# Kernel optimization log

Hardware: AMD Instinct MI355X
Metric: run time of the kernel (lower is better)

The kernel has to match this reference:

```python
import jax, jax.numpy as jnp
import numpy as np

SHIFTS = (1, 2, 4, 8)  # exponential strategy, num_shifts=4

B, L, D = 2, 2048, 2048
CAT = D * (1 + 2 * len(SHIFTS))  # 18432


def setup_inputs() -> dict:
    key = jax.random.key(0)
    kx, kw, kb = jax.random.split(key, 3)
    x = jax.random.normal(kx, (B, L, D), dtype=jnp.float32)
    # nn.Linear(cat_dim, dim_out) weight is [dim_out, cat_dim]; store as [cat_dim, dim_out] transposed for matmul
    W = jax.random.normal(kw, (D, CAT), dtype=jnp.float32) * (1.0 / np.sqrt(CAT))
    b = jax.random.normal(kb, (D,), dtype=jnp.float32) * 0.01
    return {"x": x, "W": W, "b": b}


def reference(x, W, b):
    # x: [B, L, D]; W: [dim_out, cat_dim]; b: [dim_out]
    glo = jnp.mean(x, axis=1, keepdims=True)  # [B, 1, D] global context
    feats = [jax.nn.silu(x)]
    for s in SHIFTS:
        rg = jnp.roll(glo, s, axis=-1)          # [B, 1, D]
        xg = x * rg                              # [B, L, D]
        feats.append(jax.nn.silu(xg))            # inner(s)
        rx = jnp.roll(x, s, axis=-1)
        feats.append(xg - rx * glo)              # wedge(s)
    mixed = jnp.concatenate(feats, axis=-1)      # [B, L, cat_dim]
    out = jnp.einsum('blc,oc->blo', mixed, W) + b
    return out
```

## Files before the change

kernel.cpp:

```cpp
#include <hip/hip_runtime.h>
#include <stdint.h>

#define DDIM 2048
#define LDIM 2048
#define BDIM 2
#define CATK 18432
#define MDIM 4096
#define NDIM 2048
#define KGEMM 12288
#define KCHUNK 6144

typedef short bf16x8 __attribute__((ext_vector_type(8)));
typedef float f32x4 __attribute__((ext_vector_type(4)));
typedef unsigned short u16x8 __attribute__((ext_vector_type(8)));

__device__ __forceinline__ unsigned short f2bf(float f) {
  uint32_t u = __float_as_uint(f);
  return (unsigned short)((u + 0x7fffu + ((u >> 16) & 1u)) >> 16);
}
__device__ __forceinline__ float silu_f(float v) { return v / (1.0f + __expf(-v)); }

__device__ __forceinline__ void async16(const void* g, void* l) {
  __builtin_amdgcn_global_load_lds(
      (const __attribute__((address_space(1))) uint32_t*)(uintptr_t)g,
      (__attribute__((address_space(3))) uint32_t*)(uintptr_t)l, 16, 0, 0);
}

__global__ __launch_bounds__(256) void glo_partial(const float* __restrict__ x,
                                                   float* __restrict__ part) {
  int g = blockIdx.x;
  int dc = g & 7, sl = (g >> 3) & 15, b = g >> 7;
  int d = dc * 256 + threadIdx.x;
  const float* p = x + ((size_t)b * LDIM + (size_t)sl * 128) * DDIM + d;
  float s = 0.f;
  #pragma unroll 8
  for (int i = 0; i < 128; ++i) s += p[(size_t)i * DDIM];
  part[(size_t)(b * 16 + sl) * DDIM + d] = s;
}

__global__ __launch_bounds__(256) void glo_final(const float* __restrict__ part,
                                                 float* __restrict__ glo) {
  int idx = blockIdx.x * 256 + threadIdx.x;
  int b = idx >> 11, d = idx & 2047;
  float s = 0.f;
  #pragma unroll
  for (int i = 0; i < 16; ++i) s += part[(size_t)(b * 16 + i) * DDIM + d];
  glo[idx] = s * (1.0f / (float)LDIM);
}

__global__ __launch_bounds__(256) void conv_w5(const float* __restrict__ W,
                                               unsigned short* __restrict__ Wcat) {
  int k = blockIdx.x;
  int o = blockIdx.y;
  int srcb = (k == 0) ? 0 : (2 * k - 1);
  const float* src = W + (size_t)o * CATK + srcb * 2048 + threadIdx.x * 8;
  f32x4 a = *(const f32x4*)src;
  f32x4 c = *(const f32x4*)(src + 4);
  u16x8 v;
  v[0] = f2bf(a[0]); v[1] = f2bf(a[1]); v[2] = f2bf(a[2]); v[3] = f2bf(a[3]);
  v[4] = f2bf(c[0]); v[5] = f2bf(c[1]); v[6] = f2bf(c[2]); v[7] = f2bf(c[3]);
  size_t dst = (size_t)o * KGEMM + k * 2048 + threadIdx.x * 8;
  *(u16x8*)(Wcat + dst) = v;
  *(u16x8*)(Wcat + (size_t)2048 * KGEMM + dst) = v;
}

__global__ __launch_bounds__(256) void fold_w(const float* __restrict__ W,
                                              const float* __restrict__ glo,
                                              unsigned short* __restrict__ Wcat) {
  __shared__ float ws[4][2048];
  __shared__ float gsh[2048];
  int o = blockIdx.x, b = blockIdx.y;
  const float* gb = glo + (size_t)b * 2048;
  for (int i = threadIdx.x; i < 512; i += 256) {
    *(f32x4*)&gsh[i * 4] = *(const f32x4*)&gb[i * 4];
    #pragma unroll
    for (int j = 0; j < 4; ++j)
      *(f32x4*)&ws[j][i * 4] =
          *(const f32x4*)(W + (size_t)o * CATK + (2 + 2 * j) * 2048 + i * 4);
  }
  __syncthreads();
  int d0 = threadIdx.x * 8;
  u16x8 out;
  #pragma unroll
  for (int e = 0; e < 8; ++e) {
    int d = d0 + e;
    float v = 0.f;
    #pragma unroll
    for (int j = 0; j < 4; ++j) {
      int s = 1 << j;
      int dm = (d - s) & 2047, dp = (d + s) & 2047;
      v += ws[j][d] * gsh[dm] - ws[j][dp] * gsh[dp];
    }
    out[e] = f2bf(v);
  }
  *(u16x8*)(Wcat + ((size_t)b * 2048 + o) * KGEMM + 10240 + d0) = out;
}

__global__ __launch_bounds__(256) void build_mixed(const float* __restrict__ x,
                                                   const float* __restrict__ glo,
                                                   unsigned short* __restrict__ mixed) {
  __shared__ float xs[DDIM];
  __shared__ float gs[DDIM];
  int row = blockIdx.x;
  int b = row >> 11;
  const float* xr = x + (size_t)row * DDIM;
  const float* gr = glo + (size_t)b * DDIM;
  for (int i = threadIdx.x; i < DDIM / 4; i += 256) {
    *(f32x4*)&xs[i * 4] = *(const f32x4*)&xr[i * 4];
    *(f32x4*)&gs[i * 4] = *(const f32x4*)&gr[i * 4];
  }
  __syncthreads();
  unsigned short* mr = mixed + (size_t)row * KGEMM;
  int d0 = threadIdx.x * 8;
  u16x8 o0, oi[4], xb;
  #pragma unroll
  for (int j = 0; j < 8; ++j) {
    int d = d0 + j;
    float xv = xs[d];
    o0[j] = f2bf(silu_f(xv));
    xb[j] = f2bf(xv);
    #pragma unroll
    for (int si = 0; si < 4; ++si) {
      int s = 1 << si;
      int dm = (d - s) & (DDIM - 1);
      oi[si][j] = f2bf(silu_f(xv * gs[dm]));
    }
  }
  *(u16x8*)(mr + d0) = o0;
  #pragma unroll
  for (int si = 0; si < 4; ++si)
    *(u16x8*)(mr + (size_t)(1 + si) * DDIM + d0) = oi[si];
  *(u16x8*)(mr + (size_t)10240 + d0) = xb;
}

#define BAR() __builtin_amdgcn_s_barrier()
#define SCHEDB() __builtin_amdgcn_sched_barrier(0)
#define WAIT_VM4() asm volatile("s_waitcnt vmcnt(4)" ::: "memory")
#define WAIT_VM0() asm volatile("s_waitcnt vmcnt(0)" ::: "memory")
#define WAIT_LGKM0() asm volatile("s_waitcnt lgkmcnt(0)" ::: "memory")

#define STAGE_A(S, H, KREL)                                            \
  do {                                                                 \
    const unsigned short* g_ = gA + (size_t)((H)*128) * KGEMM + (KREL);\
    unsigned short* l_ = stA + ((S)*2 + (H)) * 8192;                   \
    async16(g_, l_);                                                   \
    async16(g_ + (size_t)8 * KGEMM, l_ + 512);                         \
  } while (0)

#define STAGE_B(S, H, KREL)                                            \
  do {                                                                 \
    const unsigned short* g_ = gB + (size_t)((H)*128) * KGEMM + (KREL);\
    unsigned short* l_ = stB + ((S)*2 + (H)) * 8192;                   \
    async16(g_, l_);                                                   \
    async16(g_ + (size_t)8 * KGEMM, l_ + 512);                         \
  } while (0)

#define LOAD_A(S, MH)                                                        \
  do {                                                                       \
    _Pragma("unroll") for (int mi = 0; mi < 4; ++mi) {                       \
      ra[mi][0] = *(const bf16x8*)(pA + (S)*16384 + ((MH)*64 + mi*16)*64 + sl0); \
      ra[mi][1] = *(const bf16x8*)(pA + (S)*16384 + ((MH)*64 + mi*16)*64 + sl1); \
    }                                                                        \
  } while (0)

#define LOAD_B(S, NH, RB)                                                    \
  do {                                                                       \
    _Pragma("unroll") for (int nj = 0; nj < 2; ++nj) {                       \
      RB[nj][0] = *(const bf16x8*)(pB + (S)*16384 + ((NH)*32 + nj*16)*64 + sl0); \
      RB[nj][1] = *(const bf16x8*)(pB + (S)*16384 + ((NH)*32 + nj*16)*64 + sl1); \
    }                                                                        \
  } while (0)

#define MFMA_QUAD(MH, NH, RB)                                                \
  do {                                                                       \
    __builtin_amdgcn_s_setprio(1);                                           \
    _Pragma("unroll") for (int kk = 0; kk < 2; ++kk)                         \
      _Pragma("unroll") for (int mi = 0; mi < 4; ++mi)                       \
        _Pragma("unroll") for (int nj = 0; nj < 2; ++nj)                     \
          acc[(MH)*4 + mi][(NH)*2 + nj] = __builtin_amdgcn_mfma_f32_16x16x32_bf16( \
              ra[mi][kk], RB[nj][kk], acc[(MH)*4 + mi][(NH)*2 + nj], 0, 0, 0);     \
    __builtin_amdgcn_s_setprio(0);                                           \
  } while (0)

__global__ __launch_bounds__(512, 2) void gemm256(const unsigned short* __restrict__ A,
                                                  const unsigned short* __restrict__ Bw,
                                                  const float* __restrict__ bias,
                                                  float* __restrict__ out0,
                                                  float* __restrict__ out1) {
  extern __shared__ unsigned short lds[];
  unsigned short* ldsA = lds;
  unsigned short* ldsB = lds + 32768;

  int bid = blockIdx.x;
  int swz = (bid & 7) * 32 + (bid >> 3);
  int kc = swz >> 7;
  int rem = swz & 127;
  int mt = rem >> 3, nt = rem & 7;
  size_t kbase = (size_t)kc * KCHUNK;

  int tid = threadIdx.x;
  int wave = tid >> 6, lane = tid & 63;
  int wr = wave >> 2, wcol = wave & 3;
  int lrow = lane & 15, kq = lane >> 4, r3 = lrow & 7;
  int rIn8 = lane >> 3;
  int scOff = ((lane & 7) ^ rIn8) * 8;
  int wv16 = wave * 16;

  const unsigned short* gA = A + (size_t)(mt * 256 + wv16 + rIn8) * KGEMM + kbase + scOff;
  const unsigned short* gB = Bw + (size_t)(mt >= 8 ? 2048 : 0) * KGEMM +
                             (size_t)(nt * 256 + wv16 + rIn8) * KGEMM + kbase + scOff;
  unsigned short* stA = ldsA + wv16 * 64;
  unsigned short* stB = ldsB + wv16 * 64;

  const unsigned short* pA = ldsA + wr * 8192 + lrow * 64;
  const unsigned short* pB = ldsB + (wcol >> 1) * 8192 + ((wcol & 1) * 64 + lrow) * 64;
  int sl0 = (kq ^ r3) * 8, sl1 = ((kq + 4) ^ r3) * 8;

  f32x4 acc[8][4];
  #pragma unroll
  for (int i = 0; i < 8; ++i)
    #pragma unroll
    for (int j = 0; j < 4; ++j) acc[i][j] = (f32x4)0.f;
  bf16x8 ra[4][2], rb0[2][2], rb1[2][2];

  STAGE_B(0, 0, 0); STAGE_B(0, 1, 0);
  STAGE_A(0, 0, 0); STAGE_A(0, 1, 0);
  STAGE_B(1, 0, 64); STAGE_B(1, 1, 64);
  WAIT_VM4(); SCHEDB();
  BAR(); SCHEDB();

  for (int t = 0; t < 47; ++t) {
    size_t k0 = (size_t)t * 128;
    LOAD_A(0, 0); LOAD_B(0, 0, rb0);
    STAGE_A(1, 0, k0 + 64);
    BAR(); WAIT_LGKM0(); SCHEDB();
    MFMA_QUAD(0, 0, rb0);
    SCHEDB(); BAR(); SCHEDB();
    LOAD_B(0, 1, rb1);
    STAGE_A(1, 1, k0 + 64);
    BAR(); WAIT_LGKM0(); SCHEDB();
    MFMA_QUAD(0, 1, rb1);
    SCHEDB(); BAR(); SCHEDB();
    LOAD_A(0, 1);
    STAGE_B(0, 0, k0 + 128);
    BAR(); WAIT_LGKM0(); SCHEDB();
    MFMA_QUAD(1, 1, rb1);
    SCHEDB(); BAR(); SCHEDB();
    STAGE_B(0, 1, k0 + 128);
    BAR(); SCHEDB();
    MFMA_QUAD(1, 0, rb0);
    WAIT_VM4(); SCHEDB(); BAR(); SCHEDB();
    LOAD_A(1, 0); LOAD_B(1, 0, rb0);
    STAGE_A(0, 0, k0 + 128);
    BAR(); WAIT_LGKM0(); SCHEDB();
    MFMA_QUAD(0, 0, rb0);
    SCHEDB(); BAR(); SCHEDB();
    LOAD_B(1, 1, rb1);
    STAGE_A(0, 1, k0 + 128);
    BAR(); WAIT_LGKM0(); SCHEDB();
    MFMA_QUAD(0, 1, rb1);
    SCHEDB(); BAR(); SCHEDB();
    LOAD_A(1, 1);
    STAGE_B(1, 0, k0 + 192);
    BAR(); WAIT_LGKM0(); SCHEDB();
    MFMA_QUAD(1, 1, rb1);
    SCHEDB(); BAR(); SCHEDB();
    STAGE_B(1, 1, k0 + 192);
    BAR(); SCHEDB();
    MFMA_QUAD(1, 0, rb0);
    WAIT_VM4(); SCHEDB(); BAR(); SCHEDB();
  }

  {
    size_t k0 = (size_t)47 * 128;
    LOAD_A(0, 0); LOAD_B(0, 0, rb0);
    STAGE_A(1, 0, k0 + 64);
    BAR(); WAIT_LGKM0(); SCHEDB();
    MFMA_QUAD(0, 0, rb0);
    SCHEDB(); BAR(); SCHEDB();
    LOAD_B(0, 1, rb1);
    STAGE_A(1, 1, k0 + 64);
    BAR(); WAIT_LGKM0(); SCHEDB();
    MFMA_QUAD(0, 1, rb1);
    SCHEDB(); BAR(); SCHEDB();
    LOAD_A(0, 1);
    BAR(); WAIT_LGKM0(); SCHEDB();
    MFMA_QUAD(1, 1, rb1);
    SCHEDB(); BAR(); SCHEDB();
    BAR(); SCHEDB();
    MFMA_QUAD(1, 0, rb0);
    WAIT_VM0(); SCHEDB(); BAR(); SCHEDB();
    LOAD_A(1, 0); LOAD_B(1, 0, rb0);
    BAR(); WAIT_LGKM0(); SCHEDB();
    MFMA_QUAD(0, 0, rb0);
    SCHEDB(); BAR(); SCHEDB();
    LOAD_B(1, 1, rb1);
    BAR(); WAIT_LGKM0(); SCHEDB();
    MFMA_QUAD(0, 1, rb1);
    SCHEDB(); BAR(); SCHEDB();
    LOAD_A(1, 1);
    BAR(); WAIT_LGKM0(); SCHEDB();
    MFMA_QUAD(1, 1, rb1);
    SCHEDB(); BAR(); SCHEDB();
    MFMA_QUAD(1, 0, rb0);
  }

  float* dst = kc ? out1 : out0;
  float bv[4];
  #pragma unroll
  for (int J = 0; J < 4; ++J)
    bv[J] = kc ? 0.f : bias[nt * 256 + wcol * 64 + J * 16 + lrow];
  #pragma unroll
  for (int I = 0; I < 8; ++I) {
    int row0 = mt * 256 + wr * 128 + I * 16 + kq * 4;
    #pragma unroll
    for (int J = 0; J < 4; ++J) {
      int col = nt * 256 + wcol * 64 + J * 16 + lrow;
      #pragma unroll
      for (int r = 0; r < 4; ++r)
        dst[(size_t)(row0 + r) * NDIM + col] = acc[I][J][r] + bv[J];
    }
  }
}

__global__ __launch_bounds__(256) void combine(float* __restrict__ out,
                                               const float* __restrict__ p1) {
  size_t n = (size_t)MDIM * NDIM / 4;
  size_t stride = (size_t)gridDim.x * 256;
  for (size_t i = (size_t)blockIdx.x * 256 + threadIdx.x; i < n; i += stride) {
    f32x4 a = ((const f32x4*)out)[i];
    f32x4 c = ((const f32x4*)p1)[i];
    ((f32x4*)out)[i] = a + c;
  }
}

extern "C" void kernel_launch(void* const* d_in, const int* in_sizes, int n_in,
                              void* d_out, int out_size, void* d_ws, size_t ws_size,
                              hipStream_t stream) {
  const float* x = (const float*)d_in[0];
  const float* W = (const float*)d_in[1];
  const float* b = (const float*)d_in[2];
  float* out = (float*)d_out;

  uint8_t* ws = (uint8_t*)d_ws;
  size_t offWcat = 0;
  size_t szWcat = (size_t)2 * NDIM * KGEMM * 2;
  size_t offMx = offWcat + szWcat;
  size_t szMx = (size_t)MDIM * KGEMM * 2;
  size_t offGlo = offMx + szMx;
  size_t szGlo = (size_t)BDIM * DDIM * 4;
  size_t offPart = offGlo + szGlo;
  size_t szPart = (size_t)BDIM * 16 * DDIM * 4;
  size_t offP1 = offPart + szPart;
  size_t szP1 = (size_t)MDIM * NDIM * 4;
  if (ws_size < offP1 + szP1) return;

  unsigned short* Wcat = (unsigned short*)(ws + offWcat);
  unsigned short* Mx = (unsigned short*)(ws + offMx);
  float* glo = (float*)(ws + offGlo);
  float* part = (float*)(ws + offPart);
  float* P1 = (float*)(ws + offP1);

  hipFuncSetAttribute((const void*)gemm256, hipFuncAttributeMaxDynamicSharedMemorySize,
                      131072);

  hipLaunchKernelGGL(glo_partial, dim3(256), dim3(256), 0, stream, x, part);
  hipLaunchKernelGGL(glo_final, dim3(16), dim3(256), 0, stream, part, glo);
  hipLaunchKernelGGL(conv_w5, dim3(5, 2048), dim3(256), 0, stream, W, Wcat);
  hipLaunchKernelGGL(fold_w, dim3(2048, 2), dim3(256), 0, stream, W, glo, Wcat);
  hipLaunchKernelGGL(build_mixed, dim3(4096), dim3(256), 0, stream, x, glo, Mx);

  hipLaunchKernelGGL(gemm256, dim3(256), dim3(512), 131072, stream, Mx, Wcat, b, out, P1);
  hipLaunchKernelGGL(combine, dim3(2048), dim3(256), 0, stream, out, P1);
}
```

Baseline: 295.5 us.

## Burst all LDS fragment reads per stage and merge fold_w batches

The GEMM main loop now issues all A and B fragment reads from LDS at the start of each stage into separate register sets (raA, raB, rb0, rb1). It then waits with partial lgkmcnt counts (12, 8, 0) so MFMAs can start while later reads are still in flight, replacing the serialized load-wait-compute steps. Separately, fold_w handles both batches in one block, so each W slice is read from memory once instead of twice. The extra fragment registers raise register pressure under the 512-thread, 2-block launch bound, and the partial-wait counts depend on how the compiler orders the LDS reads.

```diff
diff --git a/kernel.cpp b/kernel.cpp
--- a/kernel.cpp
+++ b/kernel.cpp
@@ -68,11 +68,11 @@
                                               const float* __restrict__ glo,
                                               unsigned short* __restrict__ Wcat) {
   __shared__ float ws[4][2048];
-  __shared__ float gsh[2048];
-  int o = blockIdx.x, b = blockIdx.y;
-  const float* gb = glo + (size_t)b * 2048;
+  __shared__ float g2[2][2048];
+  int o = blockIdx.x;
   for (int i = threadIdx.x; i < 512; i += 256) {
-    *(f32x4*)&gsh[i * 4] = *(const f32x4*)&gb[i * 4];
+    *(f32x4*)&g2[0][i * 4] = *(const f32x4*)&glo[i * 4];
+    *(f32x4*)&g2[1][i * 4] = *(const f32x4*)&glo[2048 + i * 4];
     #pragma unroll
     for (int j = 0; j < 4; ++j)
       *(f32x4*)&ws[j][i * 4] =
@@ -80,20 +80,23 @@
   }
   __syncthreads();
   int d0 = threadIdx.x * 8;
-  u16x8 out;
-  #pragma unroll
-  for (int e = 0; e < 8; ++e) {
-    int d = d0 + e;
-    float v = 0.f;
-    #pragma unroll
-    for (int j = 0; j < 4; ++j) {
-      int s = 1 << j;
-      int dm = (d - s) & 2047, dp = (d + s) & 2047;
-      v += ws[j][d] * gsh[dm] - ws[j][dp] * gsh[dp];
+  #pragma unroll
+  for (int b = 0; b < 2; ++b) {
+    u16x8 outv;
+    #pragma unroll
+    for (int e = 0; e < 8; ++e) {
+      int d = d0 + e;
+      float v = 0.f;
+      #pragma unroll
+      for (int j = 0; j < 4; ++j) {
+        int s = 1 << j;
+        int dm = (d - s) & 2047, dp = (d + s) & 2047;
+        v += ws[j][d] * g2[b][dm] - ws[j][dp] * g2[b][dp];
+      }
+      outv[e] = f2bf(v);
     }
-    out[e] = f2bf(v);
-  }
-  *(u16x8*)(Wcat + ((size_t)b * 2048 + o) * KGEMM + 10240 + d0) = out;
+    *(u16x8*)(Wcat + ((size_t)b * 2048 + o) * KGEMM + 10240 + d0) = outv;
+  }
 }
 
 __global__ __launch_bounds__(256) void build_mixed(const float* __restrict__ x,
@@ -137,7 +140,7 @@
 #define SCHEDB() __builtin_amdgcn_sched_barrier(0)
 #define WAIT_VM4() asm volatile("s_waitcnt vmcnt(4)" ::: "memory")
 #define WAIT_VM0() asm volatile("s_waitcnt vmcnt(0)" ::: "memory")
-#define WAIT_LGKM0() asm volatile("s_waitcnt lgkmcnt(0)" ::: "memory")
+#define WAIT_LGKM(N) asm volatile("s_waitcnt lgkmcnt(" #N ")" ::: "memory")
 
 #define STAGE_A(S, H, KREL)                                            \
   do {                                                                 \
@@ -155,11 +158,11 @@
     async16(g_ + (size_t)8 * KGEMM, l_ + 512);                         \
   } while (0)
 
-#define LOAD_A(S, MH)                                                        \
+#define LOAD_A(S, MH, RA)                                                    \
   do {                                                                       \
     _Pragma("unroll") for (int mi = 0; mi < 4; ++mi) {                       \
-      ra[mi][0] = *(const bf16x8*)(pA + (S)*16384 + ((MH)*64 + mi*16)*64 + sl0); \
-      ra[mi][1] = *(const bf16x8*)(pA + (S)*16384 + ((MH)*64 + mi*16)*64 + sl1); \
+      RA[mi][0] = *(const bf16x8*)(pA + (S)*16384 + ((MH)*64 + mi*16)*64 + sl0); \
+      RA[mi][1] = *(const bf16x8*)(pA + (S)*16384 + ((MH)*64 + mi*16)*64 + sl1); \
     }                                                                        \
   } while (0)
 
@@ -171,15 +174,23 @@
     }                                                                        \
   } while (0)
 
-#define MFMA_QUAD(MH, NH, RB)                                                \
+#define MFMA_QUAD(MH, NH, RA, RB)                                            \
   do {                                                                       \
     __builtin_amdgcn_s_setprio(1);                                           \
     _Pragma("unroll") for (int kk = 0; kk < 2; ++kk)                         \
       _Pragma("unroll") for (int mi = 0; mi < 4; ++mi)                       \
         _Pragma("unroll") for (int nj = 0; nj < 2; ++nj)                     \
           acc[(MH)*4 + mi][(NH)*2 + nj] = __builtin_amdgcn_mfma_f32_16x16x32_bf16( \
-              ra[mi][kk], RB[nj][kk], acc[(MH)*4 + mi][(NH)*2 + nj], 0, 0, 0);     \
+              RA[mi][kk], RB[nj][kk], acc[(MH)*4 + mi][(NH)*2 + nj], 0, 0, 0);     \
     __builtin_amdgcn_s_setprio(0);                                           \
+  } while (0)
+
+#define BURST_READS(S)                                                       \
+  do {                                                                       \
+    LOAD_A(S, 0, raA); SCHEDB();                                             \
+    LOAD_B(S, 0, rb0); SCHEDB();                                             \
+    LOAD_B(S, 1, rb1); SCHEDB();                                             \
+    LOAD_A(S, 1, raB); SCHEDB();                                             \
   } while (0)
 
 __global__ __launch_bounds__(512, 2) void gemm256(const unsigned short* __restrict__ A,
@@ -221,7 +232,7 @@
   for (int i = 0; i < 8; ++i)
     #pragma unroll
     for (int j = 0; j < 4; ++j) acc[i][j] = (f32x4)0.f;
-  bf16x8 ra[4][2], rb0[2][2], rb1[2][2];
+  bf16x8 raA[4][2], raB[4][2], rb0[2][2], rb1[2][2];
 
   STAGE_B(0, 0, 0); STAGE_B(0, 1, 0);
   STAGE_A(0, 0, 0); STAGE_A(0, 1, 0);
@@ -231,78 +242,70 @@
 
   for (int t = 0; t < 47; ++t) {
     size_t k0 = (size_t)t * 128;
-    LOAD_A(0, 0); LOAD_B(0, 0, rb0);
+    BURST_READS(0);
     STAGE_A(1, 0, k0 + 64);
-    BAR(); WAIT_LGKM0(); SCHEDB();
-    MFMA_QUAD(0, 0, rb0);
-    SCHEDB(); BAR(); SCHEDB();
-    LOAD_B(0, 1, rb1);
+    BAR(); WAIT_LGKM(12); SCHEDB();
+    MFMA_QUAD(0, 0, raA, rb0);
+    SCHEDB(); BAR(); SCHEDB();
     STAGE_A(1, 1, k0 + 64);
-    BAR(); WAIT_LGKM0(); SCHEDB();
-    MFMA_QUAD(0, 1, rb1);
-    SCHEDB(); BAR(); SCHEDB();
-    LOAD_A(0, 1);
+    BAR(); WAIT_LGKM(8); SCHEDB();
+    MFMA_QUAD(0, 1, raA, rb1);
+    SCHEDB(); BAR(); SCHEDB();
     STAGE_B(0, 0, k0 + 128);
-    BAR(); WAIT_LGKM0(); SCHEDB();
-    MFMA_QUAD(1, 1, rb1);
+    BAR(); WAIT_LGKM(0); SCHEDB();
+    MFMA_QUAD(1, 1, raB, rb1);
     SCHEDB(); BAR(); SCHEDB();
     STAGE_B(0, 1, k0 + 128);
     BAR(); SCHEDB();
-    MFMA_QUAD(1, 0, rb0);
+    MFMA_QUAD(1, 0, raB, rb0);
     WAIT_VM4(); SCHEDB(); BAR(); SCHEDB();
-    LOAD_A(1, 0); LOAD_B(1, 0, rb0);
+    BURST_READS(1);
     STAGE_A(0, 0, k0 + 128);
-    BAR(); WAIT_LGKM0(); SCHEDB();
-    MFMA_QUAD(0, 0, rb0);
-    SCHEDB(); BAR(); SCHEDB();
-    LOAD_B(1, 1, rb1);
+    BAR(); WAIT_LGKM(12); SCHEDB();
+    MFMA_QUAD(0, 0, raA, rb0);
+    SCHEDB(); BAR(); SCHEDB();
     STAGE_A(0, 1, k0 + 128);
-    BAR(); WAIT_LGKM0(); SCHEDB();
-    MFMA_QUAD(0, 1, rb1);
-    SCHEDB(); BAR(); SCHEDB();
-    LOAD_A(1, 1);
+    BAR(); WAIT_LGKM(8); SCHEDB();
+    MFMA_QUAD(0, 1, raA, rb1);
+    SCHEDB(); BAR(); SCHEDB();
     STAGE_B(1, 0, k0 + 192);
-    BAR(); WAIT_LGKM0(); SCHEDB();
-    MFMA_QUAD(1, 1, rb1);
+    BAR(); WAIT_LGKM(0); SCHEDB();
+    MFMA_QUAD(1, 1, raB, rb1);
     SCHEDB(); BAR(); SCHEDB();
     STAGE_B(1, 1, k0 + 192);
     BAR(); SCHEDB();
-    MFMA_QUAD(1, 0, rb0);
+    MFMA_QUAD(1, 0, raB, rb0);
     WAIT_VM4(); SCHEDB(); BAR(); SCHEDB();
   }
 
   {
     size_t k0 = (size_t)47 * 128;
-    LOAD_A(0, 0); LOAD_B(0, 0, rb0);
+    BURST_READS(0);
     STAGE_A(1, 0, k0 + 64);
-    BAR(); WAIT_LGKM0(); SCHEDB();
-    MFMA_QUAD(0, 0, rb0);
-    SCHEDB(); BAR(); SCHEDB();
-    LOAD_B(0, 1, rb1);
+    BAR(); WAIT_LGKM(12); SCHEDB();
+    MFMA_QUAD(0, 0, raA, rb0);
+    SCHEDB(); BAR(); SCHEDB();
     STAGE_A(1, 1, k0 + 64);
-    BAR(); WAIT_LGKM0(); SCHEDB();
-    MFMA_QUAD(0, 1, rb1);
-    SCHEDB(); BAR(); SCHEDB();
-    LOAD_A(0, 1);
-    BAR(); WAIT_LGKM0(); SCHEDB();
-    MFMA_QUAD(1, 1, rb1);
+    BAR(); WAIT_LGKM(8); SCHEDB();
+    MFMA_QUAD(0, 1, raA, rb1);
+    SCHEDB(); BAR(); SCHEDB();
+    BAR(); WAIT_LGKM(0); SCHEDB();
+    MFMA_QUAD(1, 1, raB, rb1);
     SCHEDB(); BAR(); SCHEDB();
     BAR(); SCHEDB();
-    MFMA_QUAD(1, 0, rb0);
+    MFMA_QUAD(1, 0, raB, rb0);
     WAIT_VM0(); SCHEDB(); BAR(); SCHEDB();
-    LOAD_A(1, 0); LOAD_B(1, 0, rb0);
-    BAR(); WAIT_LGKM0(); SCHEDB();
-    MFMA_QUAD(0, 0, rb0);
-    SCHEDB(); BAR(); SCHEDB();
-    LOAD_B(1, 1, rb1);
-    BAR(); WAIT_LGKM0(); SCHEDB();
-    MFMA_QUAD(0, 1, rb1);
-    SCHEDB(); BAR(); SCHEDB();
-    LOAD_A(1, 1);
-    BAR(); WAIT_LGKM0(); SCHEDB();
-    MFMA_QUAD(1, 1, rb1);
-    SCHEDB(); BAR(); SCHEDB();
-    MFMA_QUAD(1, 0, rb0);
+    BURST_READS(1);
+    BAR(); WAIT_LGKM(12); SCHEDB();
+    MFMA_QUAD(0, 0, raA, rb0);
+    SCHEDB(); BAR(); SCHEDB();
+    BAR(); WAIT_LGKM(8); SCHEDB();
+    MFMA_QUAD(0, 1, raA, rb1);
+    SCHEDB(); BAR(); SCHEDB();
+    BAR(); WAIT_LGKM(0); SCHEDB();
+    MFMA_QUAD(1, 1, raB, rb1);
+    SCHEDB(); BAR(); SCHEDB();
+    MFMA_QUAD(1, 0, raB, rb0);
   }
 
   float* dst = kc ? out1 : out0;
@@ -367,7 +370,7 @@
   hipLaunchKernelGGL(glo_partial, dim3(256), dim3(256), 0, stream, x, part);
   hipLaunchKernelGGL(glo_final, dim3(16), dim3(256), 0, stream, part, glo);
   hipLaunchKernelGGL(conv_w5, dim3(5, 2048), dim3(256), 0, stream, W, Wcat);
-  hipLaunchKernelGGL(fold_w, dim3(2048, 2), dim3(256), 0, stream, W, glo, Wcat);
+  hipLaunchKernelGGL(fold_w, dim3(2048), dim3(256), 0, stream, W, glo, Wcat);
   hipLaunchKernelGGL(build_mixed, dim3(4096), dim3(256), 0, stream, x, glo, Mx);
 
   hipLaunchKernelGGL(gemm256, dim3(256), dim3(512), 131072, stream, Mx, Wcat, b, out, P1);
```

New measurement: 283.4 us. 1.04x faster.
